# Kernel optimization log

Hardware: AMD Instinct MI355X
Metric: run time of the kernel (lower is better)

## Reference

```python
import jax, jax.numpy as jnp
import numpy as np

N_NODES = 50000
N_EDGES = 800000
H = 128
CHEM_DIM = 34   # 2 + 2*num_gdf
GEOM_DIM = 48   # 2*num_gdf + num_signatures
EPS = 1e-5


def _linear_params(key, d_in, d_out):
    kw, kb = jax.random.split(key)
    lim = 1.0 / np.sqrt(d_in)
    w = jax.random.uniform(kw, (d_in, d_out), jnp.float32, -lim, lim)
    b = jax.random.uniform(kb, (d_out,), jnp.float32, -lim, lim)
    return w, b


def setup_inputs() -> dict:
    key = jax.random.key(0)
    ks = jax.random.split(key, 16)
    inp = {
        'chem_feats': jax.random.normal(ks[0], (N_EDGES, CHEM_DIM), jnp.float32),
        'geom_feats': jax.random.normal(ks[1], (N_NODES, GEOM_DIM), jnp.float32),
        'nbr_vids': jax.random.randint(ks[2], (N_EDGES,), 0, N_NODES, jnp.int32),
    }
    # chem_mlp: Linear(34,128) -> BN(128) -> SiLU -> Linear(128,256) -> BN(256)
    inp['w_c1'], inp['b_c1'] = _linear_params(ks[3], CHEM_DIM, H)
    inp['g_c1'], inp['be_c1'] = jnp.ones((H,), jnp.float32), jnp.zeros((H,), jnp.float32)
    inp['w_c2'], inp['b_c2'] = _linear_params(ks[4], H, 2 * H)
    inp['g_c2'], inp['be_c2'] = jnp.ones((2 * H,), jnp.float32), jnp.zeros((2 * H,), jnp.float32)
    # geom_mlp: Linear(48,64) -> BN(64) -> SiLU -> Linear(64,64) -> BN(64)
    inp['w_g1'], inp['b_g1'] = _linear_params(ks[5], GEOM_DIM, H // 2)
    inp['g_g1'], inp['be_g1'] = jnp.ones((H // 2,), jnp.float32), jnp.zeros((H // 2,), jnp.float32)
    inp['w_g2'], inp['b_g2'] = _linear_params(ks[6], H // 2, H // 2)
    inp['g_g2'], inp['be_g2'] = jnp.ones((H // 2,), jnp.float32), jnp.zeros((H // 2,), jnp.float32)
    # feat_mlp: Linear(192,128) -> BN(128) -> SiLU -> Linear(128,128) -> BN(128)
    inp['w_f1'], inp['b_f1'] = _linear_params(ks[7], H + H // 2, H)
    inp['g_f1'], inp['be_f1'] = jnp.ones((H,), jnp.float32), jnp.zeros((H,), jnp.float32)
    inp['w_f2'], inp['b_f2'] = _linear_params(ks[8], H, H)
    inp['g_f2'], inp['be_f2'] = jnp.ones((H,), jnp.float32), jnp.zeros((H,), jnp.float32)
    return inp


def _bn(x, gamma, beta):
    # BatchNorm1d with batch statistics (training-mode normalization; dropout = identity at eval)
    m = jnp.mean(x, axis=0)
    v = jnp.var(x, axis=0)
    return gamma * (x - m) * jax.lax.rsqrt(v + EPS) + beta


def reference(chem_feats, geom_feats, nbr_vids,
              w_c1, b_c1, g_c1, be_c1, w_c2, b_c2, g_c2, be_c2,
              w_g1, b_g1, g_g1, be_g1, w_g2, b_g2, g_g2, be_g2,
              w_f1, b_f1, g_f1, be_f1, w_f2, b_f2, g_f2, be_f2):
    # chem branch: per-edge MLP
    h = _bn(chem_feats @ w_c1 + b_c1, g_c1, be_c1)
    h = jax.nn.silu(h)
    h = _bn(h @ w_c2 + b_c2, g_c2, be_c2)            # [E, 2H]
    nbr_filter, nbr_core = jnp.split(h, 2, axis=-1)
    h_chem = jax.nn.sigmoid(nbr_filter) * jax.nn.softplus(nbr_core)  # [E, H]
    # scatter-sum per-edge features into node bins
    h_chem = jax.ops.segment_sum(h_chem, nbr_vids, num_segments=N_NODES)  # [N, H]
    # geom branch: per-node MLP
    hg = _bn(geom_feats @ w_g1 + b_g1, g_g1, be_g1)
    hg = jax.nn.silu(hg)
    h_geom = _bn(hg @ w_g2 + b_g2, g_g2, be_g2)      # [N, H/2]
    # fuse
    hf = jnp.concatenate((h_chem, h_geom), axis=-1)  # [N, 3H/2]
    hf = _bn(hf @ w_f1 + b_f1, g_f1, be_f1)
    hf = jax.nn.silu(hf)
    h_out = _bn(hf @ w_f2 + b_f2, g_f2, be_f2)       # [N, H]
    return h_out
```

## Files before the change

kernel.cpp:

```cpp
#include <hip/hip_runtime.h>
#include <hip/hip_bf16.h>
#include <cmath>

#define E_EDGES 800000
#define N_NODES 50000
#define BN_EPS 1e-5f

typedef __attribute__((ext_vector_type(8))) short short8;
typedef __attribute__((ext_vector_type(4))) float float4v;
typedef unsigned short ushort_t;

#define MFMA16(a, b, c) __builtin_amdgcn_mfma_f32_16x16x32_bf16((a), (b), (c), 0, 0, 0)

#define OFF_GX 0
#define OFF_GH 2304
#define OFF_A1 23040
#define OFF_C1 23168
#define OFF_A2 23296
#define OFF_C2 23552
#define OFF_GS1SUM 23808
#define OFF_GS1SQ 23872
#define OFF_GS2SUM 23936
#define OFF_GS2SQ 24000
#define OFF_FS1SUM 24064
#define OFF_FS1SQ 24192
#define OFF_FS2SUM 24320
#define OFF_FS2SQ 24448
#define OFF_NODE 24576
#define OFF_TG2 (OFF_NODE + N_NODES * 128)
#define OFF_TF1 (OFF_TG2 + N_NODES * 64)
#define OFF_TF2 OFF_NODE
#define OFF_W1T (OFF_TF1 + N_NODES * 128)
#define OFF_W2T (OFF_W1T + 4096)

__device__ __forceinline__ float frcp_(float x) { return __builtin_amdgcn_rcpf(x); }
__device__ __forceinline__ float sigmoid_(float x) { return frcp_(1.0f + __expf(-x)); }
__device__ __forceinline__ float softplus_(float x) {
  return (x > 20.0f) ? x : __logf(1.0f + __expf(x));
}
__device__ __forceinline__ float silu_(float x) { return x * frcp_(1.0f + __expf(-x)); }

__device__ __forceinline__ ushort_t f2bf(float f) {
  __hip_bfloat16 h = __float2bfloat16(f);
  return *(ushort_t*)&h;
}
__device__ __forceinline__ float bf2f(ushort_t u) {
  return __uint_as_float(((unsigned)u) << 16);
}

__device__ __forceinline__ void load_xfrag(const float* __restrict__ chem, int e, int qd,
                                           short8* x0, short8* x1) {
  const float* xe = chem + e * 34;
  float2 p0 = *(const float2*)(xe + 8 * qd);
  float2 p1 = *(const float2*)(xe + 8 * qd + 2);
  float2 p2 = *(const float2*)(xe + 8 * qd + 4);
  float2 p3 = *(const float2*)(xe + 8 * qd + 6);
  short8 a;
  a[0] = (short)f2bf(p0.x); a[1] = (short)f2bf(p0.y);
  a[2] = (short)f2bf(p1.x); a[3] = (short)f2bf(p1.y);
  a[4] = (short)f2bf(p2.x); a[5] = (short)f2bf(p2.y);
  a[6] = (short)f2bf(p3.x); a[7] = (short)f2bf(p3.y);
  *x0 = a;
  short8 b = (short8){0, 0, 0, 0, 0, 0, 0, 0};
  if (qd == 0) {
    float2 pt = *(const float2*)(xe + 32);
    b[0] = (short)f2bf(pt.x); b[1] = (short)f2bf(pt.y);
  }
  *x1 = b;
}

__global__ __launch_bounds__(256) void k_prep(const float* __restrict__ w1,
                                              const float* __restrict__ w2,
                                              float* __restrict__ ws) {
  ushort_t* w1t = (ushort_t*)(ws + OFF_W1T);
  ushort_t* w2t = (ushort_t*)(ws + OFF_W2T);
  int idx = blockIdx.x * 256 + threadIdx.x;
  if (idx < 128 * 64) {
    int c = idx >> 6, k = idx & 63;
    float v = (k < 34) ? w1[k * 128 + c] : 0.0f;
    w1t[idx] = f2bf(v);
  }
  int j = idx - 128 * 64;
  if (j >= 0 && j < 256 * 128) {
    int c = j >> 7, k = j & 127;
    w2t[j] = f2bf(w2[k * 256 + c]);
  }
}

__global__ __launch_bounds__(256) void k_xstats(const float* __restrict__ chem,
                                                float* __restrict__ ws) {
  __shared__ __align__(16) ushort_t xT[2][48 * 72];
  const int t = threadIdx.x, wv = t >> 6, ln = t & 63, r15 = ln & 15, qd = ln >> 4;
  for (int i = t; i < 2 * 14 * 72; i += 256) {
    int b = i / (14 * 72), j = i % (14 * 72);
    int rr = j / 72, e = j % 72;
    xT[b][(34 + rr) * 72 + e] = (rr == 0 && e < 64) ? f2bf(1.0f) : (ushort_t)0;
  }
  float4v g0 = {0, 0, 0, 0}, g1 = {0, 0, 0, 0};
#pragma unroll 2
  for (int it = 0; it < 10; ++it) {
    const int st = blockIdx.x * 10 + it;
    const int buf = it & 1;
    for (int i = t; i < 64 * 34; i += 256) {
      int e = i / 34, k = i - e * 34;
      xT[buf][k * 72 + e] = f2bf(chem[st * 2176 + i]);
    }
    __syncthreads();
    const ushort_t* xb = &xT[buf][0];
#pragma unroll
    for (int ks = 0; ks < 2; ++ks) {
      const ushort_t* xk = xb + ks * 32 + 8 * qd;
      short8 f0 = *(const short8*)&xk[(0 + r15) * 72];
      short8 f1 = *(const short8*)&xk[(16 + r15) * 72];
      short8 f2v = *(const short8*)&xk[(32 + r15) * 72];
      if (wv == 0) { g0 = MFMA16(f0, f0, g0); g1 = MFMA16(f0, f1, g1); }
      else if (wv == 1) { g0 = MFMA16(f0, f2v, g0); g1 = MFMA16(f1, f1, g1); }
      else if (wv == 2) { g0 = MFMA16(f1, f2v, g0); }
      else { g0 = MFMA16(f2v, f2v, g0); }
    }
  }
  float* GX = ws + OFF_GX;
  int ti0, tj0, ti1 = -1, tj1 = -1;
  if (wv == 0) { ti0 = 0; tj0 = 0; ti1 = 0; tj1 = 1; }
  else if (wv == 1) { ti0 = 0; tj0 = 2; ti1 = 1; tj1 = 1; }
  else if (wv == 2) { ti0 = 1; tj0 = 2; }
  else { ti0 = 2; tj0 = 2; }
#pragma unroll
  for (int r = 0; r < 4; ++r)
    atomicAdd(&GX[(16 * ti0 + 4 * qd + r) * 48 + 16 * tj0 + r15], g0[r]);
  if (ti1 >= 0)
#pragma unroll
    for (int r = 0; r < 4; ++r)
      atomicAdd(&GX[(16 * ti1 + 4 * qd + r) * 48 + 16 * tj1 + r15], g1[r]);
}

__global__ __launch_bounds__(64) void k_bn1(const float* __restrict__ b1,
                                            const float* __restrict__ g1,
                                            const float* __restrict__ be1,
                                            float* __restrict__ ws) {
  const int c = blockIdx.x, i = threadIdx.x;
  __shared__ float wc[34];
  const ushort_t* w1t = (const ushort_t*)(ws + OFF_W1T);
  const float* GX = ws + OFF_GX;
  if (i < 34) wc[i] = bf2f(w1t[c * 64 + i]);
  __syncthreads();
  float p = 0.0f, ps = 0.0f;
  if (i < 34) {
    float gi = 0.0f;
    for (int j = 0; j < 34; ++j) {
      int a = i, b = j;
      if ((a >> 4) > (b >> 4)) { int tt = a; a = b; b = tt; }
      gi += GX[a * 48 + b] * wc[j];
    }
    p = wc[i] * gi;
    ps = wc[i] * GX[i * 48 + 34];
  }
#pragma unroll
  for (int off = 1; off < 64; off <<= 1) {
    p += __shfl_xor(p, off);
    ps += __shfl_xor(ps, off);
  }
  if (i == 0) {
    const float E = (float)E_EDGES;
    float bc = b1[c];
    float sum = ps + E * bc;
    float sq = p + 2.0f * bc * ps + E * bc * bc;
    float m = sum / E, v = sq / E - m * m;
    float a = g1[c] * rsqrtf(v + BN_EPS);
    ws[OFF_A1 + c] = a;
    ws[OFF_C1 + c] = a * (bc - m) + be1[c];
  }
}

template <int TJA, int TJB>
__device__ __forceinline__ void ghstep(const ushort_t* hk, int r15, float4v (&g)[11]) {
  short8 f[TJB + 1];
#pragma unroll
  for (int i = 0; i <= TJB; ++i) f[i] = *(const short8*)&hk[(16 * i + r15) * 72];
  short8 f8 = *(const short8*)&hk[(128 + r15) * 72];
  int s = 0;
#pragma unroll
  for (int ti = 0; ti <= TJA; ++ti) { g[s] = MFMA16(f[ti], f[TJA], g[s]); ++s; }
  g[s] = MFMA16(f8, f[TJA], g[s]); ++s;
#pragma unroll
  for (int ti = 0; ti <= TJB; ++ti) { g[s] = MFMA16(f[ti], f[TJB], g[s]); ++s; }
  g[s] = MFMA16(f8, f[TJB], g[s]);
}

__device__ __forceinline__ void ghtile(float* GH, int ti, int tj, int r15, int qd,
                                       const float4v v) {
#pragma unroll
  for (int r = 0; r < 4; ++r)
    atomicAdd(&GH[(16 * ti + 4 * qd + r) * 144 + 16 * tj + r15], v[r]);
}

template <int TJA, int TJB>
__device__ __forceinline__ void ghflush(float* GH, int r15, int qd, const float4v (&g)[11]) {
  int s = 0;
#pragma unroll
  for (int ti = 0; ti <= TJA; ++ti) { ghtile(GH, ti, TJA, r15, qd, g[s]); ++s; }
  ghtile(GH, 8, TJA, r15, qd, g[s]); ++s;
#pragma unroll
  for (int ti = 0; ti <= TJB; ++ti) { ghtile(GH, ti, TJB, r15, qd, g[s]); ++s; }
  ghtile(GH, 8, TJB, r15, qd, g[s]);
}

__global__ __launch_bounds__(256) void k_h(const float* __restrict__ chem,
                                           float* __restrict__ ws) {
  __shared__ __align__(16) ushort_t hT[2][144 * 72];
  const int t = threadIdx.x, wv = t >> 6, ln = t & 63, r15 = ln & 15, qd = ln >> 4;
  const ushort_t* w1t = (const ushort_t*)(ws + OFF_W1T);
  for (int i = t; i < 2 * 16 * 72; i += 256) {
    int b = i / (16 * 72), j = i % (16 * 72);
    int rr = j / 72, e = j % 72;
    hT[b][(128 + rr) * 72 + e] = (rr == 0 && e < 64) ? f2bf(1.0f) : (ushort_t)0;
  }
  float a1c[2], c1c[2];
#pragma unroll
  for (int cf = 0; cf < 2; ++cf) {
    int col = 32 * wv + 16 * cf + r15;
    a1c[cf] = ws[OFF_A1 + col];
    c1c[cf] = ws[OFF_C1 + col];
  }
  float4v gacc[11];
#pragma unroll
  for (int s = 0; s < 11; ++s) gacc[s] = (float4v){0, 0, 0, 0};

#pragma unroll 2
  for (int it = 0; it < 10; ++it) {
    const int st = blockIdx.x * 10 + it;
    const int buf = it & 1;
    const int e_base = st * 64;
    short8 xa0[4], xa1[4];
#pragma unroll
    for (int rb = 0; rb < 4; ++rb)
      load_xfrag(chem, e_base + 16 * rb + r15, qd, &xa0[rb], &xa1[rb]);
#pragma unroll
    for (int cf = 0; cf < 2; ++cf) {
      const int col = 32 * wv + 16 * cf + r15;
      short8 wb0 = *(const short8*)&w1t[col * 64 + 8 * qd];
      short8 wb1 = *(const short8*)&w1t[col * 64 + 32 + 8 * qd];
#pragma unroll
      for (int rb = 0; rb < 4; ++rb) {
        float4v acc = (float4v){0, 0, 0, 0};
        acc = MFMA16(xa0[rb], wb0, acc);
        acc = MFMA16(xa1[rb], wb1, acc);
        unsigned long long pk = 0;
#pragma unroll
        for (int r = 0; r < 4; ++r) {
          float hv = silu_(fmaf(a1c[cf], acc[r], c1c[cf]));
          pk |= ((unsigned long long)f2bf(hv)) << (16 * r);
        }
        *(unsigned long long*)&hT[buf][col * 72 + 16 * rb + 4 * qd] = pk;
      }
    }
    __syncthreads();
    const ushort_t* hb = &hT[buf][0];
#pragma unroll
    for (int ks = 0; ks < 2; ++ks) {
      const ushort_t* hk = hb + ks * 32 + 8 * qd;
      if (wv == 0) ghstep<0, 7>(hk, r15, gacc);
      else if (wv == 1) ghstep<1, 6>(hk, r15, gacc);
      else if (wv == 2) ghstep<2, 5>(hk, r15, gacc);
      else ghstep<3, 4>(hk, r15, gacc);
    }
  }
  float* GH = ws + OFF_GH;
  if (wv == 0) ghflush<0, 7>(GH, r15, qd, gacc);
  else if (wv == 1) ghflush<1, 6>(GH, r15, qd, gacc);
  else if (wv == 2) ghflush<2, 5>(GH, r15, qd, gacc);
  else ghflush<3, 4>(GH, r15, qd, gacc);
}

__global__ __launch_bounds__(128) void k_bn2(const float* __restrict__ b2,
                                             const float* __restrict__ g2,
                                             const float* __restrict__ be2,
                                             float* __restrict__ ws) {
  const int c = blockIdx.x, i = threadIdx.x;
  __shared__ float wcol[128];
  __shared__ float redQ[2], redS[2];
  const ushort_t* w2t = (const ushort_t*)(ws + OFF_W2T);
  const float* GH = ws + OFF_GH;
  wcol[i] = bf2f(w2t[c * 128 + i]);
  __syncthreads();
  float wi = wcol[i];
  float gi = 0.0f;
  for (int j = 0; j < 128; ++j) {
    int a = i, b = j;
    if ((a >> 4) > (b >> 4)) { int tt = a; a = b; b = tt; }
    gi += GH[a * 144 + b] * wcol[j];
  }
  float p = wi * gi;
  float ps = wi * GH[128 * 144 + i];
#pragma unroll
  for (int off = 1; off < 64; off <<= 1) {
    p += __shfl_xor(p, off);
    ps += __shfl_xor(ps, off);
  }
  const int wv = i >> 6, ln = i & 63;
  if (ln == 0) { redQ[wv] = p; redS[wv] = ps; }
  __syncthreads();
  if (i == 0) {
    float q = redQ[0] + redQ[1], s = redS[0] + redS[1];
    const float E = (float)E_EDGES;
    float bc = b2[c];
    float sum = s + E * bc;
    float sq = q + 2.0f * bc * s + E * bc * bc;
    float m = sum / E, v = sq / E - m * m;
    float a = g2[c] * rsqrtf(v + BN_EPS);
    ws[OFF_A2 + c] = a;
    ws[OFF_C2 + c] = a * (bc - m) + be2[c];
  }
}

__global__ __launch_bounds__(256) void k_scatter(const float* __restrict__ chem,
                                                 const int* __restrict__ vids,
                                                 float* __restrict__ ws) {
  __shared__ __align__(16) ushort_t hS[2][64 * 136];
  const int t = threadIdx.x, wv = t >> 6, ln = t & 63, r15 = ln & 15, qd = ln >> 4;
  const ushort_t* w1t = (const ushort_t*)(ws + OFF_W1T);
  const ushort_t* w2t = (const ushort_t*)(ws + OFF_W2T);
  float* node = ws + OFF_NODE;
  float a1c[2], c1c[2], aF2[2], cF2[2], aC2[2], cC2[2];
#pragma unroll
  for (int cf = 0; cf < 2; ++cf) {
    int col = 32 * wv + 16 * cf + r15;
    a1c[cf] = ws[OFF_A1 + col];
    c1c[cf] = ws[OFF_C1 + col];
    aF2[cf] = ws[OFF_A2 + col];
    cF2[cf] = ws[OFF_C2 + col];
    aC2[cf] = ws[OFF_A2 + 128 + col];
    cC2[cf] = ws[OFF_C2 + 128 + col];
  }
#pragma unroll 2
  for (int it = 0; it < 8; ++it) {
    const int st = blockIdx.x * 8 + it;
    if (st >= 12500) break;
    const int buf = it & 1;
    const int e_base = st * 64;
    const int myvid = vids[e_base + ln];
    short8 xa0[4], xa1[4];
#pragma unroll
    for (int rb = 0; rb < 4; ++rb)
      load_xfrag(chem, e_base + 16 * rb + r15, qd, &xa0[rb], &xa1[rb]);
#pragma unroll
    for (int cf = 0; cf < 2; ++cf) {
      const int col = 32 * wv + 16 * cf + r15;
      short8 wb0 = *(const short8*)&w1t[col * 64 + 8 * qd];
      short8 wb1 = *(const short8*)&w1t[col * 64 + 32 + 8 * qd];
#pragma unroll
      for (int rb = 0; rb < 4; ++rb) {
        float4v acc = (float4v){0, 0, 0, 0};
        acc = MFMA16(xa0[rb], wb0, acc);
        acc = MFMA16(xa1[rb], wb1, acc);
#pragma unroll
        for (int r = 0; r < 4; ++r) {
          float hv = silu_(fmaf(a1c[cf], acc[r], c1c[cf]));
          hS[buf][(16 * rb + 4 * qd + r) * 136 + col] = f2bf(hv);
        }
      }
    }
    __syncthreads();
    const ushort_t* hb = &hS[buf][0];
#pragma unroll
    for (int cf = 0; cf < 2; ++cf) {
      const int colF = 32 * wv + 16 * cf + r15;
      float4v accF[4], accC[4];
#pragma unroll
      for (int rb = 0; rb < 4; ++rb) {
        accF[rb] = (float4v){0, 0, 0, 0};
        accC[rb] = (float4v){0, 0, 0, 0};
      }
#pragma unroll
      for (int ks = 0; ks < 4; ++ks) {
        short8 bF = *(const short8*)&w2t[colF * 128 + ks * 32 + 8 * qd];
        short8 bC = *(const short8*)&w2t[(128 + colF) * 128 + ks * 32 + 8 * qd];
#pragma unroll
        for (int rb = 0; rb < 4; ++rb) {
          short8 hf = *(const short8*)&hb[(16 * rb + r15) * 136 + ks * 32 + 8 * qd];
          accF[rb] = MFMA16(hf, bF, accF[rb]);
          accC[rb] = MFMA16(hf, bC, accC[rb]);
        }
      }
#pragma unroll
      for (int rb = 0; rb < 4; ++rb)
#pragma unroll
        for (int r = 0; r < 4; ++r) {
          float F = fmaf(aF2[cf], accF[rb][r], cF2[cf]);
          float Co = fmaf(aC2[cf], accC[rb][r], cC2[cf]);
          float gv = sigmoid_(F) * softplus_(Co);
          int vid = __shfl(myvid, 16 * rb + 4 * qd + r);
          atomicAdd(node + (size_t)vid * 128 + colF, gv);
        }
    }
  }
}

__global__ __launch_bounds__(256) void k_geom_stats1(const float* __restrict__ geom,
                                                     const float* __restrict__ wg1,
                                                     const float* __restrict__ bg1,
                                                     float* __restrict__ ws) {
  __shared__ float ssum[64], ssq[64];
  const int t = threadIdx.x, lane = t & 63, w = t >> 6;
  if (t < 64) { ssum[t] = 0.0f; ssq[t] = 0.0f; }
  __syncthreads();
  const float bcol = bg1[lane];
  const int nb = blockIdx.x * 16 + w * 4;
  float x[4], acc[4];
#pragma unroll
  for (int u = 0; u < 4; u++) {
    x[u] = (lane < 48) ? geom[(nb + u) * 48 + lane] : 0.0f;
    acc[u] = bcol;
  }
#pragma unroll 16
  for (int k = 0; k < 48; k++) {
    float wvv = wg1[k * 64 + lane];
#pragma unroll
    for (int u = 0; u < 4; u++) acc[u] = fmaf(__shfl(x[u], k), wvv, acc[u]);
  }
  float bs = 0.0f, bq = 0.0f;
#pragma unroll
  for (int u = 0; u < 4; u++) { bs += acc[u]; bq += acc[u] * acc[u]; }
  atomicAdd(&ssum[lane], bs);
  atomicAdd(&ssq[lane], bq);
  __syncthreads();
  if (t < 64) {
    atomicAdd(ws + OFF_GS1SUM + t, ssum[t]);
    atomicAdd(ws + OFF_GS1SQ + t, ssq[t]);
  }
}

__global__ __launch_bounds__(256) void k_geom_main(
    const float* __restrict__ geom, const float* __restrict__ wg1,
    const float* __restrict__ bg1, const float* __restrict__ gg1,
    const float* __restrict__ beg1, const float* __restrict__ wg2,
    const float* __restrict__ bg2, float* __restrict__ ws) {
  __shared__ float ssum[64], ssq[64];
  const int t = threadIdx.x, lane = t & 63, w = t >> 6;
  if (t < 64) { ssum[t] = 0.0f; ssq[t] = 0.0f; }
  const float invN = 1.0f / (float)N_NODES;
  float s1 = ws[OFF_GS1SUM + lane], q1 = ws[OFF_GS1SQ + lane];
  float m1 = s1 * invN, v1 = q1 * invN - m1 * m1;
  float a1 = gg1[lane] * rsqrtf(v1 + BN_EPS);
  float c1 = beg1[lane] - a1 * m1;
  const float bcol = bg1[lane], b2col = bg2[lane];
  __syncthreads();
  const int nb = blockIdx.x * 16 + w * 4;
  float x[4], tg1[4], hg[4], acc[4];
#pragma unroll
  for (int u = 0; u < 4; u++) {
    x[u] = (lane < 48) ? geom[(nb + u) * 48 + lane] : 0.0f;
    tg1[u] = bcol;
  }
#pragma unroll 16
  for (int k = 0; k < 48; k++) {
    float wvv = wg1[k * 64 + lane];
#pragma unroll
    for (int u = 0; u < 4; u++) tg1[u] = fmaf(__shfl(x[u], k), wvv, tg1[u]);
  }
#pragma unroll
  for (int u = 0; u < 4; u++) {
    hg[u] = silu_(fmaf(a1, tg1[u], c1));
    acc[u] = b2col;
  }
#pragma unroll 16
  for (int k = 0; k < 64; k++) {
    float wvv = wg2[k * 64 + lane];
#pragma unroll
    for (int u = 0; u < 4; u++) acc[u] = fmaf(__shfl(hg[u], k), wvv, acc[u]);
  }
  float bs = 0.0f, bq = 0.0f;
#pragma unroll
  for (int u = 0; u < 4; u++) {
    ws[OFF_TG2 + (nb + u) * 64 + lane] = acc[u];
    bs += acc[u]; bq += acc[u] * acc[u];
  }
  atomicAdd(&ssum[lane], bs);
  atomicAdd(&ssq[lane], bq);
  __syncthreads();
  if (t < 64) {
    atomicAdd(ws + OFF_GS2SUM + t, ssum[t]);
    atomicAdd(ws + OFF_GS2SQ + t, ssq[t]);
  }
}

__global__ __launch_bounds__(256) void k_fuse1(const float* __restrict__ wf1,
                                               const float* __restrict__ bf1,
                                               const float* __restrict__ gg2,
                                               const float* __restrict__ beg2,
                                               float* __restrict__ ws) {
  __shared__ float ssum[128], ssq[128];
  const int t = threadIdx.x, lane = t & 63, w = t >> 6;
  if (t < 128) { ssum[t] = 0.0f; ssq[t] = 0.0f; }
  const float invN = 1.0f / (float)N_NODES;
  float s2 = ws[OFF_GS2SUM + lane], q2 = ws[OFF_GS2SQ + lane];
  float mg = s2 * invN, vg = q2 * invN - mg * mg;
  float ag = gg2[lane] * rsqrtf(vg + BN_EPS);
  float cg_ = beg2[lane] - ag * mg;
  const float bA = bf1[lane], bB = bf1[64 + lane];
  __syncthreads();
  const int nb = blockIdx.x * 16 + w * 4;
  float xa[4], xb[4], xg[4], acc1[4], acc2[4];
#pragma unroll
  for (int u = 0; u < 4; u++) {
    int n = nb + u;
    xa[u] = ws[OFF_NODE + n * 128 + lane];
    xb[u] = ws[OFF_NODE + n * 128 + 64 + lane];
    xg[u] = fmaf(ag, ws[OFF_TG2 + n * 64 + lane], cg_);
    acc1[u] = bA; acc2[u] = bB;
  }
#pragma unroll 16
  for (int k = 0; k < 64; k++) {
    float w1v = wf1[k * 128 + lane], w2v = wf1[k * 128 + 64 + lane];
#pragma unroll
    for (int u = 0; u < 4; u++) {
      float xk = __shfl(xa[u], k);
      acc1[u] = fmaf(xk, w1v, acc1[u]);
      acc2[u] = fmaf(xk, w2v, acc2[u]);
    }
  }
#pragma unroll 16
  for (int k = 0; k < 64; k++) {
    float w1v = wf1[(64 + k) * 128 + lane], w2v = wf1[(64 + k) * 128 + 64 + lane];
#pragma unroll
    for (int u = 0; u < 4; u++) {
      float xk = __shfl(xb[u], k);
      acc1[u] = fmaf(xk, w1v, acc1[u]);
      acc2[u] = fmaf(xk, w2v, acc2[u]);
    }
  }
#pragma unroll 16
  for (int k = 0; k < 64; k++) {
    float w1v = wf1[(128 + k) * 128 + lane], w2v = wf1[(128 + k) * 128 + 64 + lane];
#pragma unroll
    for (int u = 0; u < 4; u++) {
      float xk = __shfl(xg[u], k);
      acc1[u] = fmaf(xk, w1v, acc1[u]);
      acc2[u] = fmaf(xk, w2v, acc2[u]);
    }
  }
  float sA = 0, qA = 0, sB = 0, qB = 0;
#pragma unroll
  for (int u = 0; u < 4; u++) {
    int n = nb + u;
    ws[OFF_TF1 + n * 128 + lane] = acc1[u];
    ws[OFF_TF1 + n * 128 + 64 + lane] = acc2[u];
    sA += acc1[u]; qA += acc1[u] * acc1[u];
    sB += acc2[u]; qB += acc2[u] * acc2[u];
  }
  atomicAdd(&ssum[lane], sA); atomicAdd(&ssq[lane], qA);
  atomicAdd(&ssum[64 + lane], sB); atomicAdd(&ssq[64 + lane], qB);
  __syncthreads();
  if (t < 128) {
    atomicAdd(ws + OFF_FS1SUM + t, ssum[t]);
    atomicAdd(ws + OFF_FS1SQ + t, ssq[t]);
  }
}

__global__ __launch_bounds__(256) void k_fuse2(const float* __restrict__ wf2,
                                               const float* __restrict__ bf2,
                                               const float* __restrict__ gf1,
                                               const float* __restrict__ bef1,
                                               float* __restrict__ ws) {
  __shared__ float ssum[128], ssq[128];
  const int t = threadIdx.x, lane = t & 63, w = t >> 6;
  if (t < 128) { ssum[t] = 0.0f; ssq[t] = 0.0f; }
  const float invN = 1.0f / (float)N_NODES;
  float sA_ = ws[OFF_FS1SUM + lane], qA_ = ws[OFF_FS1SQ + lane];
  float mA = sA_ * invN, vA = qA_ * invN - mA * mA;
  float aA = gf1[lane] * rsqrtf(vA + BN_EPS);
  float cA = bef1[lane] - aA * mA;
  float sB_ = ws[OFF_FS1SUM + 64 + lane], qB_ = ws[OFF_FS1SQ + 64 + lane];
  float mB = sB_ * invN, vB = qB_ * invN - mB * mB;
  float aB = gf1[64 + lane] * rsqrtf(vB + BN_EPS);
  float cB = bef1[64 + lane] - aB * mB;
  const float b1c = bf2[lane], b2c = bf2[64 + lane];
  __syncthreads();
  const int nb = blockIdx.x * 16 + w * 4;
  float ha[4], hb[4], acc1[4], acc2[4];
#pragma unroll
  for (int u = 0; u < 4; u++) {
    int n = nb + u;
    ha[u] = silu_(fmaf(aA, ws[OFF_TF1 + n * 128 + lane], cA));
    hb[u] = silu_(fmaf(aB, ws[OFF_TF1 + n * 128 + 64 + lane], cB));
    acc1[u] = b1c; acc2[u] = b2c;
  }
#pragma unroll 16
  for (int k = 0; k < 64; k++) {
    float w1v = wf2[k * 128 + lane], w2v = wf2[k * 128 + 64 + lane];
#pragma unroll
    for (int u = 0; u < 4; u++) {
      float xk = __shfl(ha[u], k);
      acc1[u] = fmaf(xk, w1v, acc1[u]);
      acc2[u] = fmaf(xk, w2v, acc2[u]);
    }
  }
#pragma unroll 16
  for (int k = 0; k < 64; k++) {
    float w1v = wf2[(64 + k) * 128 + lane], w2v = wf2[(64 + k) * 128 + 64 + lane];
#pragma unroll
    for (int u = 0; u < 4; u++) {
      float xk = __shfl(hb[u], k);
      acc1[u] = fmaf(xk, w1v, acc1[u]);
      acc2[u] = fmaf(xk, w2v, acc2[u]);
    }
  }
  float sA = 0, qA = 0, sB = 0, qB = 0;
#pragma unroll
  for (int u = 0; u < 4; u++) {
    int n = nb + u;
    ws[OFF_TF2 + n * 128 + lane] = acc1[u];
    ws[OFF_TF2 + n * 128 + 64 + lane] = acc2[u];
    sA += acc1[u]; qA += acc1[u] * acc1[u];
    sB += acc2[u]; qB += acc2[u] * acc2[u];
  }
  atomicAdd(&ssum[lane], sA); atomicAdd(&ssq[lane], qA);
  atomicAdd(&ssum[64 + lane], sB); atomicAdd(&ssq[64 + lane], qB);
  __syncthreads();
  if (t < 128) {
    atomicAdd(ws + OFF_FS2SUM + t, ssum[t]);
    atomicAdd(ws + OFF_FS2SQ + t, ssq[t]);
  }
}

__global__ __launch_bounds__(256) void k_final(const float* __restrict__ gf2,
                                               const float* __restrict__ bef2,
                                               const float* __restrict__ ws,
                                               float* __restrict__ out) {
  const int idx = blockIdx.x * 256 + threadIdx.x;
  const int base = idx * 4;
  if (base >= N_NODES * 128) return;
  const float invN = 1.0f / (float)N_NODES;
  const int c0 = base & 127;
  float4 v = *(const float4*)(ws + OFF_TF2 + base);
  float vv[4] = {v.x, v.y, v.z, v.w}, r[4];
#pragma unroll
  for (int j = 0; j < 4; j++) {
    int c = c0 + j;
    float s = ws[OFF_FS2SUM + c], q = ws[OFF_FS2SQ + c];
    float m = s * invN, var = q * invN - m * m;
    float a = gf2[c] * rsqrtf(var + BN_EPS);
    r[j] = fmaf(a, vv[j] - m, bef2[c]);
  }
  *(float4*)(out + base) = make_float4(r[0], r[1], r[2], r[3]);
}

extern "C" void kernel_launch(void* const* d_in, const int* in_sizes, int n_in,
                              void* d_out, int out_size, void* d_ws, size_t ws_size,
                              hipStream_t stream) {
  const float* chem = (const float*)d_in[0];
  const float* geom = (const float*)d_in[1];
  const int* vids = (const int*)d_in[2];
  const float* w_c1 = (const float*)d_in[3];  const float* b_c1 = (const float*)d_in[4];
  const float* g_c1 = (const float*)d_in[5];  const float* be_c1 = (const float*)d_in[6];
  const float* w_c2 = (const float*)d_in[7];  const float* b_c2 = (const float*)d_in[8];
  const float* g_c2 = (const float*)d_in[9];  const float* be_c2 = (const float*)d_in[10];
  const float* w_g1 = (const float*)d_in[11]; const float* b_g1 = (const float*)d_in[12];
  const float* g_g1 = (const float*)d_in[13]; const float* be_g1 = (const float*)d_in[14];
  const float* w_g2 = (const float*)d_in[15]; const float* b_g2 = (const float*)d_in[16];
  const float* g_g2 = (const float*)d_in[17]; const float* be_g2 = (const float*)d_in[18];
  const float* w_f1 = (const float*)d_in[19]; const float* b_f1 = (const float*)d_in[20];
  const float* g_f1 = (const float*)d_in[21]; const float* be_f1 = (const float*)d_in[22];
  const float* w_f2 = (const float*)d_in[23]; const float* b_f2 = (const float*)d_in[24];
  const float* g_f2 = (const float*)d_in[25]; const float* be_f2 = (const float*)d_in[26];
  float* ws = (float*)d_ws;
  float* out = (float*)d_out;

  hipMemsetAsync(d_ws, 0, (size_t)(OFF_NODE + N_NODES * 128) * sizeof(float), stream);

  k_prep<<<dim3(160), dim3(256), 0, stream>>>(w_c1, w_c2, ws);
  k_xstats<<<dim3(1250), dim3(256), 0, stream>>>(chem, ws);
  k_bn1<<<dim3(128), dim3(64), 0, stream>>>(b_c1, g_c1, be_c1, ws);
  k_h<<<dim3(1250), dim3(256), 0, stream>>>(chem, ws);
  k_bn2<<<dim3(256), dim3(128), 0, stream>>>(b_c2, g_c2, be_c2, ws);
  k_scatter<<<dim3(1563), dim3(256), 0, stream>>>(chem, vids, ws);
  k_geom_stats1<<<dim3(3125), dim3(256), 0, stream>>>(geom, w_g1, b_g1, ws);
  k_geom_main<<<dim3(3125), dim3(256), 0, stream>>>(geom, w_g1, b_g1, g_g1, be_g1, w_g2, b_g2, ws);
  k_fuse1<<<dim3(3125), dim3(256), 0, stream>>>(w_f1, b_f1, g_g2, be_g2, ws);
  k_fuse2<<<dim3(3125), dim3(256), 0, stream>>>(w_f2, b_f2, g_f1, be_f1, ws);
  k_final<<<dim3(6250), dim3(256), 0, stream>>>(g_f2, be_f2, ws, out);
}
```

Measured before the change: 1.190 ms.

## Sort edges by node for segmented scatter, MFMA fuse GEMMs, Gram-based geom BN stats

Builds a counting sort of edges by destination node (count, scan, place) so the scatter kernel processes edges in node order and merges runs of equal node ids before issuing atomics. The fuse1/fuse2 per-node MLPs move from scalar shuffle-FMA loops to bf16 MFMA tiles with pre-transposed bf16 weights. The geom first-layer BN statistics are computed from a Gram matrix of the inputs instead of a full extra pass over the linear layer. This adds three small sorting kernels, a single-block scan, gathered chem loads, and bf16 rounding in the fuse layers.

```diff
diff --git a/kernel.cpp b/kernel.cpp
--- a/kernel.cpp
+++ b/kernel.cpp
@@ -9,6 +9,7 @@
 typedef __attribute__((ext_vector_type(8))) short short8;
 typedef __attribute__((ext_vector_type(4))) float float4v;
 typedef unsigned short ushort_t;
+typedef unsigned long long ull_t;
 
 #define MFMA16(a, b, c) __builtin_amdgcn_mfma_f32_16x16x32_bf16((a), (b), (c), 0, 0, 0)
 
@@ -18,20 +19,28 @@
 #define OFF_C1 23168
 #define OFF_A2 23296
 #define OFF_C2 23552
-#define OFF_GS1SUM 23808
-#define OFF_GS1SQ 23872
 #define OFF_GS2SUM 23936
 #define OFF_GS2SQ 24000
 #define OFF_FS1SUM 24064
 #define OFF_FS1SQ 24192
 #define OFF_FS2SUM 24320
 #define OFF_FS2SQ 24448
-#define OFF_NODE 24576
+#define OFF_GG 24576
+#define OFF_GA1 28672
+#define OFF_GC1 28736
+#define OFF_NODE 28800
 #define OFF_TG2 (OFF_NODE + N_NODES * 128)
 #define OFF_TF1 (OFF_TG2 + N_NODES * 64)
 #define OFF_TF2 OFF_NODE
 #define OFF_W1T (OFF_TF1 + N_NODES * 128)
 #define OFF_W2T (OFF_W1T + 4096)
+#define OFF_WF1T (OFF_W2T + 16384)
+#define OFF_WF2T (OFF_WF1T + 12288)
+
+#define OFFI_CNT 0
+#define OFFI_CUR 50048
+#define OFFI_PERM 100096
+#define OFFI_SVID 900096
 
 __device__ __forceinline__ float frcp_(float x) { return __builtin_amdgcn_rcpf(x); }
 __device__ __forceinline__ float sigmoid_(float x) { return frcp_(1.0f + __expf(-x)); }
@@ -46,6 +55,10 @@
 }
 __device__ __forceinline__ float bf2f(ushort_t u) {
   return __uint_as_float(((unsigned)u) << 16);
+}
+__device__ __forceinline__ ull_t pack4(float a, float b, float c, float d) {
+  return (ull_t)f2bf(a) | ((ull_t)f2bf(b) << 16) | ((ull_t)f2bf(c) << 32) |
+         ((ull_t)f2bf(d) << 48);
 }
 
 __device__ __forceinline__ void load_xfrag(const float* __restrict__ chem, int e, int qd,
@@ -71,20 +84,75 @@
 
 __global__ __launch_bounds__(256) void k_prep(const float* __restrict__ w1,
                                               const float* __restrict__ w2,
+                                              const float* __restrict__ wf1,
+                                              const float* __restrict__ wf2,
                                               float* __restrict__ ws) {
-  ushort_t* w1t = (ushort_t*)(ws + OFF_W1T);
-  ushort_t* w2t = (ushort_t*)(ws + OFF_W2T);
   int idx = blockIdx.x * 256 + threadIdx.x;
-  if (idx < 128 * 64) {
+  if (idx < 8192) {
     int c = idx >> 6, k = idx & 63;
-    float v = (k < 34) ? w1[k * 128 + c] : 0.0f;
-    w1t[idx] = f2bf(v);
-  }
-  int j = idx - 128 * 64;
-  if (j >= 0 && j < 256 * 128) {
-    int c = j >> 7, k = j & 127;
-    w2t[j] = f2bf(w2[k * 256 + c]);
-  }
+    ((ushort_t*)(ws + OFF_W1T))[idx] = f2bf((k < 34) ? w1[k * 128 + c] : 0.0f);
+  } else if (idx < 40960) {
+    int j = idx - 8192;
+    ((ushort_t*)(ws + OFF_W2T))[j] = f2bf(w2[(j & 127) * 256 + (j >> 7)]);
+  } else if (idx < 65536) {
+    int j = idx - 40960;
+    int c = j / 192, k = j - c * 192;
+    ((ushort_t*)(ws + OFF_WF1T))[j] = f2bf(wf1[k * 128 + c]);
+  } else if (idx < 81920) {
+    int j = idx - 65536;
+    ((ushort_t*)(ws + OFF_WF2T))[j] = f2bf(wf2[(j & 127) * 128 + (j >> 7)]);
+  }
+}
+
+__global__ __launch_bounds__(256) void k_count(const int* __restrict__ vids,
+                                               float* __restrict__ ws) {
+  int e = blockIdx.x * 256 + threadIdx.x;
+  int* cnt = (int*)(ws + OFF_TF1) + OFFI_CNT;
+  atomicAdd(&cnt[vids[e]], 1);
+}
+
+__global__ __launch_bounds__(1024) void k_scan(float* __restrict__ ws) {
+  int* cnt = (int*)(ws + OFF_TF1) + OFFI_CNT;
+  int* cur = (int*)(ws + OFF_TF1) + OFFI_CUR;
+  __shared__ int part[1024];
+  const int tid = threadIdx.x;
+  const int CH = 49;
+  const int base = tid * CH;
+  int s = 0;
+  for (int j = 0; j < CH; ++j) {
+    int idx = base + j;
+    if (idx < 50048) s += cnt[idx];
+  }
+  part[tid] = s;
+  __syncthreads();
+  int own = s;
+  for (int off = 1; off < 1024; off <<= 1) {
+    int v = 0;
+    if (tid >= off) v = part[tid - off];
+    __syncthreads();
+    part[tid] += v;
+    __syncthreads();
+  }
+  int run = part[tid] - own;
+  for (int j = 0; j < CH; ++j) {
+    int idx = base + j;
+    if (idx < 50048) {
+      cur[idx] = run;
+      run += cnt[idx];
+    }
+  }
+}
+
+__global__ __launch_bounds__(256) void k_place(const int* __restrict__ vids,
+                                               float* __restrict__ ws) {
+  int e = blockIdx.x * 256 + threadIdx.x;
+  int* cur = (int*)(ws + OFF_TF1) + OFFI_CUR;
+  int* perm = (int*)(ws + OFF_TF1) + OFFI_PERM;
+  int* svid = (int*)(ws + OFF_TF1) + OFFI_SVID;
+  int v = vids[e];
+  int slot = atomicAdd(&cur[v], 1);
+  perm[slot] = e;
+  svid[slot] = v;
 }
 
 __global__ __launch_bounds__(256) void k_xstats(const float* __restrict__ chem,
@@ -172,6 +240,92 @@
   }
 }
 
+__global__ __launch_bounds__(256) void k_ggram(const float* __restrict__ geom,
+                                               float* __restrict__ ws) {
+  __shared__ __align__(16) ushort_t xT[2][64 * 72];
+  const int t = threadIdx.x, wv = t >> 6, ln = t & 63, r15 = ln & 15, qd = ln >> 4;
+  for (int i = t; i < 2 * 15 * 72; i += 256) {
+    int b = i / (15 * 72), j = i % (15 * 72);
+    xT[b][(49 + j / 72) * 72 + (j % 72)] = 0;
+  }
+  float4v g0 = {0, 0, 0, 0}, g1 = {0, 0, 0, 0}, g2 = {0, 0, 0, 0};
+  for (int it = 0; it < 10; ++it) {
+    const int st = blockIdx.x * 10 + it;
+    if (st >= 782) break;
+    const int buf = it & 1;
+    const int nb = st * 64;
+    for (int i = t; i < 64 * 48; i += 256) {
+      int nl = i / 48, k = i - nl * 48;
+      int n = nb + nl;
+      xT[buf][k * 72 + nl] = (n < N_NODES) ? f2bf(geom[n * 48 + k]) : (ushort_t)0;
+    }
+    if (t < 64) xT[buf][48 * 72 + t] = (nb + t < N_NODES) ? f2bf(1.0f) : (ushort_t)0;
+    __syncthreads();
+    const ushort_t* xb = &xT[buf][0];
+#pragma unroll
+    for (int ks = 0; ks < 2; ++ks) {
+      const ushort_t* xk = xb + ks * 32 + 8 * qd;
+      short8 f0 = *(const short8*)&xk[(0 + r15) * 72];
+      short8 f1 = *(const short8*)&xk[(16 + r15) * 72];
+      short8 f2v = *(const short8*)&xk[(32 + r15) * 72];
+      short8 f3 = *(const short8*)&xk[(48 + r15) * 72];
+      if (wv == 0) { g0 = MFMA16(f0, f0, g0); g1 = MFMA16(f0, f1, g1); g2 = MFMA16(f0, f2v, g2); }
+      else if (wv == 1) { g0 = MFMA16(f0, f3, g0); g1 = MFMA16(f1, f1, g1); g2 = MFMA16(f1, f2v, g2); }
+      else if (wv == 2) { g0 = MFMA16(f1, f3, g0); g1 = MFMA16(f2v, f2v, g1); g2 = MFMA16(f2v, f3, g2); }
+      else { g0 = MFMA16(f3, f3, g0); }
+    }
+  }
+  float* GG = ws + OFF_GG;
+  int ti[3], tj[3], nacc;
+  if (wv == 0) { ti[0]=0; tj[0]=0; ti[1]=0; tj[1]=1; ti[2]=0; tj[2]=2; nacc=3; }
+  else if (wv == 1) { ti[0]=0; tj[0]=3; ti[1]=1; tj[1]=1; ti[2]=1; tj[2]=2; nacc=3; }
+  else if (wv == 2) { ti[0]=1; tj[0]=3; ti[1]=2; tj[1]=2; ti[2]=2; tj[2]=3; nacc=3; }
+  else { ti[0]=3; tj[0]=3; nacc=1; }
+  float4v gs[3] = {g0, g1, g2};
+  for (int s = 0; s < nacc; ++s)
+#pragma unroll
+    for (int r = 0; r < 4; ++r)
+      atomicAdd(&GG[(16 * ti[s] + 4 * qd + r) * 64 + 16 * tj[s] + r15], gs[s][r]);
+}
+
+__global__ __launch_bounds__(64) void k_gbn1(const float* __restrict__ wg1,
+                                             const float* __restrict__ bg1,
+                                             const float* __restrict__ gg1,
+                                             const float* __restrict__ beg1,
+                                             float* __restrict__ ws) {
+  const int c = blockIdx.x, i = threadIdx.x;
+  __shared__ float wc[48];
+  const float* GG = ws + OFF_GG;
+  if (i < 48) wc[i] = wg1[i * 64 + c];
+  __syncthreads();
+  float p = 0.0f, ps = 0.0f;
+  if (i < 48) {
+    float gi = 0.0f;
+    for (int j = 0; j < 48; ++j) {
+      int a = i, b = j;
+      if ((a >> 4) > (b >> 4)) { int tt = a; a = b; b = tt; }
+      gi += GG[a * 64 + b] * wc[j];
+    }
+    p = wc[i] * gi;
+    ps = wc[i] * GG[i * 64 + 48];
+  }
+#pragma unroll
+  for (int off = 1; off < 64; off <<= 1) {
+    p += __shfl_xor(p, off);
+    ps += __shfl_xor(ps, off);
+  }
+  if (i == 0) {
+    const float Nf = (float)N_NODES;
+    float bc = bg1[c];
+    float sum = ps + Nf * bc;
+    float sq = p + 2.0f * bc * ps + Nf * bc * bc;
+    float m = sum / Nf, v = sq / Nf - m * m;
+    float a = gg1[c] * rsqrtf(v + BN_EPS);
+    ws[OFF_GA1 + c] = a;
+    ws[OFF_GC1 + c] = beg1[c] - a * m;
+  }
+}
+
 template <int TJA, int TJB>
 __device__ __forceinline__ void ghstep(const ushort_t* hk, int r15, float4v (&g)[11]) {
   short8 f[TJB + 1];
@@ -245,13 +399,13 @@
         float4v acc = (float4v){0, 0, 0, 0};
         acc = MFMA16(xa0[rb], wb0, acc);
         acc = MFMA16(xa1[rb], wb1, acc);
-        unsigned long long pk = 0;
+        ull_t pk = 0;
 #pragma unroll
         for (int r = 0; r < 4; ++r) {
           float hv = silu_(fmaf(a1c[cf], acc[r], c1c[cf]));
-          pk |= ((unsigned long long)f2bf(hv)) << (16 * r);
+          pk |= ((ull_t)f2bf(hv)) << (16 * r);
         }
-        *(unsigned long long*)&hT[buf][col * 72 + 16 * rb + 4 * qd] = pk;
+        *(ull_t*)&hT[buf][col * 72 + 16 * rb + 4 * qd] = pk;
       }
     }
     __syncthreads();
@@ -314,12 +468,13 @@
 }
 
 __global__ __launch_bounds__(256) void k_scatter(const float* __restrict__ chem,
-                                                 const int* __restrict__ vids,
                                                  float* __restrict__ ws) {
   __shared__ __align__(16) ushort_t hS[2][64 * 136];
   const int t = threadIdx.x, wv = t >> 6, ln = t & 63, r15 = ln & 15, qd = ln >> 4;
   const ushort_t* w1t = (const ushort_t*)(ws + OFF_W1T);
   const ushort_t* w2t = (const ushort_t*)(ws + OFF_W2T);
+  const int* perm = (const int*)(ws + OFF_TF1) + OFFI_PERM;
+  const int* svid = (const int*)(ws + OFF_TF1) + OFFI_SVID;
   float* node = ws + OFF_NODE;
   float a1c[2], c1c[2], aF2[2], cF2[2], aC2[2], cC2[2];
 #pragma unroll
@@ -332,17 +487,20 @@
     aC2[cf] = ws[OFF_A2 + 128 + col];
     cC2[cf] = ws[OFF_C2 + 128 + col];
   }
-#pragma unroll 2
-  for (int it = 0; it < 8; ++it) {
-    const int st = blockIdx.x * 8 + it;
-    if (st >= 12500) break;
+  for (int it = 0; it < 4; ++it) {
+    const int st = blockIdx.x * 4 + it;
     const int buf = it & 1;
-    const int e_base = st * 64;
-    const int myvid = vids[e_base + ln];
+    const int s_base = st * 64;
+    int pr[4];
+    int4 vv[4];
+#pragma unroll
+    for (int rb = 0; rb < 4; ++rb) {
+      pr[rb] = perm[s_base + 16 * rb + r15];
+      vv[rb] = *(const int4*)&svid[s_base + 16 * rb + 4 * qd];
+    }
     short8 xa0[4], xa1[4];
 #pragma unroll
-    for (int rb = 0; rb < 4; ++rb)
-      load_xfrag(chem, e_base + 16 * rb + r15, qd, &xa0[rb], &xa1[rb]);
+    for (int rb = 0; rb < 4; ++rb) load_xfrag(chem, pr[rb], qd, &xa0[rb], &xa1[rb]);
 #pragma unroll
     for (int cf = 0; cf < 2; ++cf) {
       const int col = 32 * wv + 16 * cf + r15;
@@ -383,66 +541,36 @@
         }
       }
 #pragma unroll
-      for (int rb = 0; rb < 4; ++rb)
+      for (int rb = 0; rb < 4; ++rb) {
+        float gv[4];
 #pragma unroll
         for (int r = 0; r < 4; ++r) {
           float F = fmaf(aF2[cf], accF[rb][r], cF2[cf]);
           float Co = fmaf(aC2[cf], accC[rb][r], cC2[cf]);
-          float gv = sigmoid_(F) * softplus_(Co);
-          int vid = __shfl(myvid, 16 * rb + 4 * qd + r);
-          atomicAdd(node + (size_t)vid * 128 + colF, gv);
+          gv[r] = sigmoid_(F) * softplus_(Co);
         }
-    }
-  }
-}
-
-__global__ __launch_bounds__(256) void k_geom_stats1(const float* __restrict__ geom,
-                                                     const float* __restrict__ wg1,
-                                                     const float* __restrict__ bg1,
-                                                     float* __restrict__ ws) {
-  __shared__ float ssum[64], ssq[64];
-  const int t = threadIdx.x, lane = t & 63, w = t >> 6;
-  if (t < 64) { ssum[t] = 0.0f; ssq[t] = 0.0f; }
-  __syncthreads();
-  const float bcol = bg1[lane];
-  const int nb = blockIdx.x * 16 + w * 4;
-  float x[4], acc[4];
-#pragma unroll
-  for (int u = 0; u < 4; u++) {
-    x[u] = (lane < 48) ? geom[(nb + u) * 48 + lane] : 0.0f;
-    acc[u] = bcol;
-  }
-#pragma unroll 16
-  for (int k = 0; k < 48; k++) {
-    float wvv = wg1[k * 64 + lane];
-#pragma unroll
-    for (int u = 0; u < 4; u++) acc[u] = fmaf(__shfl(x[u], k), wvv, acc[u]);
-  }
-  float bs = 0.0f, bq = 0.0f;
-#pragma unroll
-  for (int u = 0; u < 4; u++) { bs += acc[u]; bq += acc[u] * acc[u]; }
-  atomicAdd(&ssum[lane], bs);
-  atomicAdd(&ssq[lane], bq);
-  __syncthreads();
-  if (t < 64) {
-    atomicAdd(ws + OFF_GS1SUM + t, ssum[t]);
-    atomicAdd(ws + OFF_GS1SQ + t, ssq[t]);
+        int cv = vv[rb].x;
+        float s = gv[0];
+        if (vv[rb].y == cv) s += gv[1];
+        else { atomicAdd(node + (size_t)cv * 128 + colF, s); cv = vv[rb].y; s = gv[1]; }
+        if (vv[rb].z == cv) s += gv[2];
+        else { atomicAdd(node + (size_t)cv * 128 + colF, s); cv = vv[rb].z; s = gv[2]; }
+        if (vv[rb].w == cv) s += gv[3];
+        else { atomicAdd(node + (size_t)cv * 128 + colF, s); cv = vv[rb].w; s = gv[3]; }
+        atomicAdd(node + (size_t)cv * 128 + colF, s);
+      }
+    }
   }
 }
 
 __global__ __launch_bounds__(256) void k_geom_main(
     const float* __restrict__ geom, const float* __restrict__ wg1,
-    const float* __restrict__ bg1, const float* __restrict__ gg1,
-    const float* __restrict__ beg1, const float* __restrict__ wg2,
+    const float* __restrict__ bg1, const float* __restrict__ wg2,
     const float* __restrict__ bg2, float* __restrict__ ws) {
   __shared__ float ssum[64], ssq[64];
   const int t = threadIdx.x, lane = t & 63, w = t >> 6;
   if (t < 64) { ssum[t] = 0.0f; ssq[t] = 0.0f; }
-  const float invN = 1.0f / (float)N_NODES;
-  float s1 = ws[OFF_GS1SUM + lane], q1 = ws[OFF_GS1SQ + lane];
-  float m1 = s1 * invN, v1 = q1 * invN - m1 * m1;
-  float a1 = gg1[lane] * rsqrtf(v1 + BN_EPS);
-  float c1 = beg1[lane] - a1 * m1;
+  const float a1 = ws[OFF_GA1 + lane], c1 = ws[OFF_GC1 + lane];
   const float bcol = bg1[lane], b2col = bg2[lane];
   __syncthreads();
   const int nb = blockIdx.x * 16 + w * 4;
@@ -484,142 +612,143 @@
   }
 }
 
-__global__ __launch_bounds__(256) void k_fuse1(const float* __restrict__ wf1,
-                                               const float* __restrict__ bf1,
+__global__ __launch_bounds__(256) void k_fuse1(const float* __restrict__ bf1,
                                                const float* __restrict__ gg2,
                                                const float* __restrict__ beg2,
                                                float* __restrict__ ws) {
-  __shared__ float ssum[128], ssq[128];
-  const int t = threadIdx.x, lane = t & 63, w = t >> 6;
-  if (t < 128) { ssum[t] = 0.0f; ssq[t] = 0.0f; }
+  __shared__ __align__(16) ushort_t zS[64 * 200];
+  __shared__ float agS[64], cgS[64];
+  const int t = threadIdx.x, wv = t >> 6, ln = t & 63, r15 = ln & 15, qd = ln >> 4;
+  const int nb = blockIdx.x * 64;
   const float invN = 1.0f / (float)N_NODES;
-  float s2 = ws[OFF_GS2SUM + lane], q2 = ws[OFF_GS2SQ + lane];
-  float mg = s2 * invN, vg = q2 * invN - mg * mg;
-  float ag = gg2[lane] * rsqrtf(vg + BN_EPS);
-  float cg_ = beg2[lane] - ag * mg;
-  const float bA = bf1[lane], bB = bf1[64 + lane];
-  __syncthreads();
-  const int nb = blockIdx.x * 16 + w * 4;
-  float xa[4], xb[4], xg[4], acc1[4], acc2[4];
-#pragma unroll
-  for (int u = 0; u < 4; u++) {
-    int n = nb + u;
-    xa[u] = ws[OFF_NODE + n * 128 + lane];
-    xb[u] = ws[OFF_NODE + n * 128 + 64 + lane];
-    xg[u] = fmaf(ag, ws[OFF_TG2 + n * 64 + lane], cg_);
-    acc1[u] = bA; acc2[u] = bB;
-  }
-#pragma unroll 16
-  for (int k = 0; k < 64; k++) {
-    float w1v = wf1[k * 128 + lane], w2v = wf1[k * 128 + 64 + lane];
-#pragma unroll
-    for (int u = 0; u < 4; u++) {
-      float xk = __shfl(xa[u], k);
-      acc1[u] = fmaf(xk, w1v, acc1[u]);
-      acc2[u] = fmaf(xk, w2v, acc2[u]);
-    }
-  }
-#pragma unroll 16
-  for (int k = 0; k < 64; k++) {
-    float w1v = wf1[(64 + k) * 128 + lane], w2v = wf1[(64 + k) * 128 + 64 + lane];
-#pragma unroll
-    for (int u = 0; u < 4; u++) {
-      float xk = __shfl(xb[u], k);
-      acc1[u] = fmaf(xk, w1v, acc1[u]);
-      acc2[u] = fmaf(xk, w2v, acc2[u]);
-    }
-  }
-#pragma unroll 16
-  for (int k = 0; k < 64; k++) {
-    float w1v = wf1[(128 + k) * 128 + lane], w2v = wf1[(128 + k) * 128 + 64 + lane];
-#pragma unroll
-    for (int u = 0; u < 4; u++) {
-      float xk = __shfl(xg[u], k);
-      acc1[u] = fmaf(xk, w1v, acc1[u]);
-      acc2[u] = fmaf(xk, w2v, acc2[u]);
-    }
-  }
-  float sA = 0, qA = 0, sB = 0, qB = 0;
-#pragma unroll
-  for (int u = 0; u < 4; u++) {
-    int n = nb + u;
-    ws[OFF_TF1 + n * 128 + lane] = acc1[u];
-    ws[OFF_TF1 + n * 128 + 64 + lane] = acc2[u];
-    sA += acc1[u]; qA += acc1[u] * acc1[u];
-    sB += acc2[u]; qB += acc2[u] * acc2[u];
-  }
-  atomicAdd(&ssum[lane], sA); atomicAdd(&ssq[lane], qA);
-  atomicAdd(&ssum[64 + lane], sB); atomicAdd(&ssq[64 + lane], qB);
-  __syncthreads();
-  if (t < 128) {
-    atomicAdd(ws + OFF_FS1SUM + t, ssum[t]);
-    atomicAdd(ws + OFF_FS1SQ + t, ssq[t]);
-  }
-}
-
-__global__ __launch_bounds__(256) void k_fuse2(const float* __restrict__ wf2,
-                                               const float* __restrict__ bf2,
+  if (t < 64) {
+    float s = ws[OFF_GS2SUM + t], q = ws[OFF_GS2SQ + t];
+    float m = s * invN, v = q * invN - m * m;
+    float a = gg2[t] * rsqrtf(v + BN_EPS);
+    agS[t] = a;
+    cgS[t] = beg2[t] - a * m;
+  }
+  __syncthreads();
+  const float* node = ws + OFF_NODE;
+  const float* tg2 = ws + OFF_TG2;
+  for (int i = t; i < 64 * 32; i += 256) {
+    int row = i >> 5, c4 = (i & 31) << 2, n = nb + row;
+    float4 v = (n < N_NODES) ? *(const float4*)&node[n * 128 + c4] : make_float4(0, 0, 0, 0);
+    *(ull_t*)&zS[row * 200 + c4] = pack4(v.x, v.y, v.z, v.w);
+  }
+  for (int i = t; i < 64 * 16; i += 256) {
+    int row = i >> 4, c4 = (i & 15) << 2, n = nb + row;
+    float4 v = (n < N_NODES) ? *(const float4*)&tg2[n * 64 + c4] : make_float4(0, 0, 0, 0);
+    float z0 = fmaf(agS[c4 + 0], v.x, cgS[c4 + 0]);
+    float z1 = fmaf(agS[c4 + 1], v.y, cgS[c4 + 1]);
+    float z2 = fmaf(agS[c4 + 2], v.z, cgS[c4 + 2]);
+    float z3 = fmaf(agS[c4 + 3], v.w, cgS[c4 + 3]);
+    *(ull_t*)&zS[row * 200 + 128 + c4] = pack4(z0, z1, z2, z3);
+  }
+  __syncthreads();
+  const ushort_t* wt = (const ushort_t*)(ws + OFF_WF1T);
+#pragma unroll
+  for (int cf = 0; cf < 2; ++cf) {
+    const int col = 32 * wv + 16 * cf + r15;
+    float4v acc[4];
+#pragma unroll
+    for (int rb = 0; rb < 4; ++rb) acc[rb] = (float4v){0, 0, 0, 0};
+#pragma unroll
+    for (int ks = 0; ks < 6; ++ks) {
+      short8 bfrag = *(const short8*)&wt[col * 192 + ks * 32 + 8 * qd];
+#pragma unroll
+      for (int rb = 0; rb < 4; ++rb) {
+        short8 afrag = *(const short8*)&zS[(16 * rb + r15) * 200 + ks * 32 + 8 * qd];
+        acc[rb] = MFMA16(afrag, bfrag, acc[rb]);
+      }
+    }
+    const float bcol = bf1[col];
+    float s = 0.0f, q = 0.0f;
+#pragma unroll
+    for (int rb = 0; rb < 4; ++rb)
+#pragma unroll
+      for (int r = 0; r < 4; ++r) {
+        int n = nb + 16 * rb + 4 * qd + r;
+        float raw = acc[rb][r] + bcol;
+        if (n < N_NODES) {
+          ws[OFF_TF1 + (size_t)n * 128 + col] = raw;
+          s += raw;
+          q += raw * raw;
+        }
+      }
+    s += __shfl_xor(s, 16); q += __shfl_xor(q, 16);
+    s += __shfl_xor(s, 32); q += __shfl_xor(q, 32);
+    if (ln < 16) {
+      atomicAdd(ws + OFF_FS1SUM + col, s);
+      atomicAdd(ws + OFF_FS1SQ + col, q);
+    }
+  }
+}
+
+__global__ __launch_bounds__(256) void k_fuse2(const float* __restrict__ bf2,
                                                const float* __restrict__ gf1,
                                                const float* __restrict__ bef1,
                                                float* __restrict__ ws) {
-  __shared__ float ssum[128], ssq[128];
-  const int t = threadIdx.x, lane = t & 63, w = t >> 6;
-  if (t < 128) { ssum[t] = 0.0f; ssq[t] = 0.0f; }
+  __shared__ __align__(16) ushort_t zS[64 * 136];
+  __shared__ float aS[128], cS[128];
+  const int t = threadIdx.x, wv = t >> 6, ln = t & 63, r15 = ln & 15, qd = ln >> 4;
+  const int nb = blockIdx.x * 64;
   const float invN = 1.0f / (float)N_NODES;
-  float sA_ = ws[OFF_FS1SUM + lane], qA_ = ws[OFF_FS1SQ + lane];
-  float mA = sA_ * invN, vA = qA_ * invN - mA * mA;
-  float aA = gf1[lane] * rsqrtf(vA + BN_EPS);
-  float cA = bef1[lane] - aA * mA;
-  float sB_ = ws[OFF_FS1SUM + 64 + lane], qB_ = ws[OFF_FS1SQ + 64 + lane];
-  float mB = sB_ * invN, vB = qB_ * invN - mB * mB;
-  float aB = gf1[64 + lane] * rsqrtf(vB + BN_EPS);
-  float cB = bef1[64 + lane] - aB * mB;
-  const float b1c = bf2[lane], b2c = bf2[64 + lane];
-  __syncthreads();
-  const int nb = blockIdx.x * 16 + w * 4;
-  float ha[4], hb[4], acc1[4], acc2[4];
-#pragma unroll
-  for (int u = 0; u < 4; u++) {
-    int n = nb + u;
-    ha[u] = silu_(fmaf(aA, ws[OFF_TF1 + n * 128 + lane], cA));
-    hb[u] = silu_(fmaf(aB, ws[OFF_TF1 + n * 128 + 64 + lane], cB));
-    acc1[u] = b1c; acc2[u] = b2c;
-  }
-#pragma unroll 16
-  for (int k = 0; k < 64; k++) {
-    float w1v = wf2[k * 128 + lane], w2v = wf2[k * 128 + 64 + lane];
-#pragma unroll
-    for (int u = 0; u < 4; u++) {
-      float xk = __shfl(ha[u], k);
-      acc1[u] = fmaf(xk, w1v, acc1[u]);
-      acc2[u] = fmaf(xk, w2v, acc2[u]);
-    }
-  }
-#pragma unroll 16
-  for (int k = 0; k < 64; k++) {
-    float w1v = wf2[(64 + k) * 128 + lane], w2v = wf2[(64 + k) * 128 + 64 + lane];
-#pragma unroll
-    for (int u = 0; u < 4; u++) {
-      float xk = __shfl(hb[u], k);
-      acc1[u] = fmaf(xk, w1v, acc1[u]);
-      acc2[u] = fmaf(xk, w2v, acc2[u]);
-    }
-  }
-  float sA = 0, qA = 0, sB = 0, qB = 0;
-#pragma unroll
-  for (int u = 0; u < 4; u++) {
-    int n = nb + u;
-    ws[OFF_TF2 + n * 128 + lane] = acc1[u];
-    ws[OFF_TF2 + n * 128 + 64 + lane] = acc2[u];
-    sA += acc1[u]; qA += acc1[u] * acc1[u];
-    sB += acc2[u]; qB += acc2[u] * acc2[u];
-  }
-  atomicAdd(&ssum[lane], sA); atomicAdd(&ssq[lane], qA);
-  atomicAdd(&ssum[64 + lane], sB); atomicAdd(&ssq[64 + lane], qB);
-  __syncthreads();
   if (t < 128) {
-    atomicAdd(ws + OFF_FS2SUM + t, ssum[t]);
-    atomicAdd(ws + OFF_FS2SQ + t, ssq[t]);
+    float s = ws[OFF_FS1SUM + t], q = ws[OFF_FS1SQ + t];
+    float m = s * invN, v = q * invN - m * m;
+    float a = gf1[t] * rsqrtf(v + BN_EPS);
+    aS[t] = a;
+    cS[t] = bef1[t] - a * m;
+  }
+  __syncthreads();
+  const float* tf1 = ws + OFF_TF1;
+  for (int i = t; i < 64 * 32; i += 256) {
+    int row = i >> 5, c4 = (i & 31) << 2, n = nb + row;
+    float4 v = (n < N_NODES) ? *(const float4*)&tf1[(size_t)n * 128 + c4] : make_float4(0, 0, 0, 0);
+    float z0 = silu_(fmaf(aS[c4 + 0], v.x, cS[c4 + 0]));
+    float z1 = silu_(fmaf(aS[c4 + 1], v.y, cS[c4 + 1]));
+    float z2 = silu_(fmaf(aS[c4 + 2], v.z, cS[c4 + 2]));
+    float z3 = silu_(fmaf(aS[c4 + 3], v.w, cS[c4 + 3]));
+    *(ull_t*)&zS[row * 136 + c4] = pack4(z0, z1, z2, z3);
+  }
+  __syncthreads();
+  const ushort_t* wt = (const ushort_t*)(ws + OFF_WF2T);
+#pragma unroll
+  for (int cf = 0; cf < 2; ++cf) {
+    const int col = 32 * wv + 16 * cf + r15;
+    float4v acc[4];
+#pragma unroll
+    for (int rb = 0; rb < 4; ++rb) acc[rb] = (float4v){0, 0, 0, 0};
+#pragma unroll
+    for (int ks = 0; ks < 4; ++ks) {
+      short8 bfrag = *(const short8*)&wt[col * 128 + ks * 32 + 8 * qd];
+#pragma unroll
+      for (int rb = 0; rb < 4; ++rb) {
+        short8 afrag = *(const short8*)&zS[(16 * rb + r15) * 136 + ks * 32 + 8 * qd];
+        acc[rb] = MFMA16(afrag, bfrag, acc[rb]);
+      }
+    }
+    const float bcol = bf2[col];
+    float s = 0.0f, q = 0.0f;
+#pragma unroll
+    for (int rb = 0; rb < 4; ++rb)
+#pragma unroll
+      for (int r = 0; r < 4; ++r) {
+        int n = nb + 16 * rb + 4 * qd + r;
+        float raw = acc[rb][r] + bcol;
+        if (n < N_NODES) {
+          ws[OFF_TF2 + (size_t)n * 128 + col] = raw;
+          s += raw;
+          q += raw * raw;
+        }
+      }
+    s += __shfl_xor(s, 16); q += __shfl_xor(q, 16);
+    s += __shfl_xor(s, 32); q += __shfl_xor(q, 32);
+    if (ln < 16) {
+      atomicAdd(ws + OFF_FS2SUM + col, s);
+      atomicAdd(ws + OFF_FS2SQ + col, q);
+    }
   }
 }
 
@@ -666,17 +795,22 @@
   float* ws = (float*)d_ws;
   float* out = (float*)d_out;
 
-  hipMemsetAsync(d_ws, 0, (size_t)(OFF_NODE + N_NODES * 128) * sizeof(float), stream);
-
-  k_prep<<<dim3(160), dim3(256), 0, stream>>>(w_c1, w_c2, ws);
+  hipMemsetAsync(d_ws, 0, (size_t)OFF_TG2 * sizeof(float), stream);
+  hipMemsetAsync((char*)d_ws + (size_t)OFF_TF1 * sizeof(float), 0, 50048 * sizeof(int), stream);
+
+  k_prep<<<dim3(320), dim3(256), 0, stream>>>(w_c1, w_c2, w_f1, w_f2, ws);
+  k_count<<<dim3(3125), dim3(256), 0, stream>>>(vids, ws);
+  k_scan<<<dim3(1), dim3(1024), 0, stream>>>(ws);
+  k_place<<<dim3(3125), dim3(256), 0, stream>>>(vids, ws);
   k_xstats<<<dim3(1250), dim3(256), 0, stream>>>(chem, ws);
   k_bn1<<<dim3(128), dim3(64), 0, stream>>>(b_c1, g_c1, be_c1, ws);
+  k_ggram<<<dim3(79), dim3(256), 0, stream>>>(geom, ws);
+  k_gbn1<<<dim3(64), dim3(64), 0, stream>>>(w_g1, b_g1, g_g1, be_g1, ws);
   k_h<<<dim3(1250), dim3(256), 0, stream>>>(chem, ws);
   k_bn2<<<dim3(256), dim3(128), 0, stream>>>(b_c2, g_c2, be_c2, ws);
-  k_scatter<<<dim3(1563), dim3(256), 0, stream>>>(chem, vids, ws);
-  k_geom_stats1<<<dim3(3125), dim3(256), 0, stream>>>(geom, w_g1, b_g1, ws);
-  k_geom_main<<<dim3(3125), dim3(256), 0, stream>>>(geom, w_g1, b_g1, g_g1, be_g1, w_g2, b_g2, ws);
-  k_fuse1<<<dim3(3125), dim3(256), 0, stream>>>(w_f1, b_f1, g_g2, be_g2, ws);
-  k_fuse2<<<dim3(3125), dim3(256), 0, stream>>>(w_f2, b_f2, g_f1, be_f1, ws);
+  k_scatter<<<dim3(3125), dim3(256), 0, stream>>>(chem, ws);
+  k_geom_main<<<dim3(3125), dim3(256), 0, stream>>>(geom, w_g1, b_g1, w_g2, b_g2, ws);
+  k_fuse1<<<dim3(782), dim3(256), 0, stream>>>(b_f1, g_g2, be_g2, ws);
+  k_fuse2<<<dim3(782), dim3(256), 0, stream>>>(b_f2, g_f1, be_f1, ws);
   k_final<<<dim3(6250), dim3(256), 0, stream>>>(g_f2, be_f2, ws, out);
 }
```

After: 1.198 ms. About the same (+0.7%).
